# Kernel tuning notes

Hardware: AMD Instinct MI355X
Metric: run time of the kernel (lower is better)

The kernel has to match this reference:

```python
import jax, jax.numpy as jnp
import numpy as np

B, S, H, NH = 4, 1024, 2048, 32
HD = H // NH
EPS = 1e-5

def layer_norm(x, w, b):
    mu = jnp.mean(x, axis=-1, keepdims=True)
    var = jnp.mean(jnp.square(x - mu), axis=-1, keepdims=True)
    return (x - mu) * jax.lax.rsqrt(var + EPS) * w + b

def setup_inputs() -> dict:
    key = jax.random.key(0)
    ks = jax.random.split(key, 8)
    s = 0.02
    inp = {
        'hidden_states': jax.random.normal(ks[0], (B, S, H), jnp.float32),
        'mask': jnp.tril(jnp.ones((S, S), jnp.float32))[None, None],  # causal 0/1
        'ln1_w': jnp.ones((H,), jnp.float32), 'ln1_b': jnp.zeros((H,), jnp.float32),
        'w_qkv': s * jax.random.normal(ks[1], (H, 3 * H), jnp.float32),
        'b_qkv': jnp.zeros((3 * H,), jnp.float32),
        'w_dense': s * jax.random.normal(ks[2], (H, H), jnp.float32),
        'b_dense': jnp.zeros((H,), jnp.float32),
        'ln3_w': jnp.ones((H,), jnp.float32), 'ln3_b': jnp.zeros((H,), jnp.float32),
        'ln2_w': jnp.ones((H,), jnp.float32), 'ln2_b': jnp.zeros((H,), jnp.float32),
        'w_h4h': s * jax.random.normal(ks[3], (H, 4 * H), jnp.float32),
        'b_h4h': jnp.zeros((4 * H,), jnp.float32),
        'w_4hh': s * jax.random.normal(ks[4], (4 * H, H), jnp.float32),
        'b_4hh': jnp.zeros((H,), jnp.float32),
        'ln4_w': jnp.ones((H,), jnp.float32), 'ln4_b': jnp.zeros((H,), jnp.float32),
    }
    return inp

def _layer(hidden_states, mask, ln1_w, ln1_b, w_qkv, b_qkv, w_dense, b_dense,
           ln3_w, ln3_b, ln2_w, ln2_b, w_h4h, b_h4h, w_4hh, b_4hh, ln4_w, ln4_b):
    # --- input LN ---
    x1 = layer_norm(hidden_states, ln1_w, ln1_b)
    # --- self attention ---
    qkv = x1 @ w_qkv + b_qkv                              # [B,S,3H]
    q, k, v = jnp.split(qkv, 3, axis=-1)
    def heads(t):  # [B,S,H] -> [B,NH,S,HD]
        return t.reshape(B, S, NH, HD).transpose(0, 2, 1, 3)
    q, k, v = heads(q), heads(k), heads(v)
    scores = jnp.einsum('bnqd,bnkd->bnqk', q / jnp.sqrt(jnp.float32(HD)), k)
    scores = scores * mask - 10000.0 * (1.0 - mask)
    probs = jax.nn.softmax(scores, axis=-1)
    ctx = jnp.einsum('bnqk,bnkd->bnqd', probs, v)
    ctx = ctx.transpose(0, 2, 1, 3).reshape(B, S, H)
    attn_out = ctx @ w_dense + b_dense
    # sandwich LN on attention output
    attn_out = layer_norm(attn_out, ln3_w, ln3_b)
    ln_input = hidden_states + attn_out
    # --- MLP ---
    x2 = layer_norm(ln_input, ln2_w, ln2_b)
    inter = jax.nn.gelu(x2 @ w_h4h + b_h4h, approximate=True)
    mlp_out = inter @ w_4hh + b_4hh
    mlp_out = layer_norm(mlp_out, ln4_w, ln4_b)
    return ln_input + mlp_out

def reference(hidden_states, mask, ln1_w, ln1_b, w_qkv, b_qkv, w_dense, b_dense,
              ln3_w, ln3_b, ln2_w, ln2_b, w_h4h, b_h4h, w_4hh, b_4hh, ln4_w, ln4_b):
    return _layer(hidden_states, mask, ln1_w, ln1_b, w_qkv, b_qkv, w_dense, b_dense,
                  ln3_w, ln3_b, ln2_w, ln2_b, w_h4h, b_h4h, w_4hh, b_4hh, ln4_w, ln4_b)
```

## Files before the change

kernel.cpp:

```cpp
#include <hip/hip_runtime.h>
#include <cstdint>
#include <cstddef>

typedef __bf16 bf16_t;
typedef __bf16 bf16x8 __attribute__((ext_vector_type(8)));
typedef float f32x4 __attribute__((ext_vector_type(4)));

#define BB 4
#define SS 1024
#define HH 2048
#define NHH 32
#define HDD 64
#define MTOK 4096
#define QKVLD 6144

static constexpr size_t OFF_WQKV   = 0;
static constexpr size_t OFF_WDENSE = 25165824;
static constexpr size_t OFF_WH4H   = 33554432;
static constexpr size_t OFF_W4HH   = 67108864;
static constexpr size_t OFF_X1     = 100663296;
static constexpr size_t OFF_QKV    = 117440512;
static constexpr size_t OFF_ATTND2 = 150994944;
static constexpr size_t OFF_VT     = 167772160;
static constexpr size_t OFF_LNIN   = 184549376;
static constexpr size_t OFF_MLP    = 218103808;
static constexpr size_t OFF_MLP2   = 0;

__device__ __forceinline__ uint16_t f2bfu(float f) {
  union { float f; uint32_t u; } v; v.f = f;
  return (uint16_t)((v.u + 0x7FFFu + ((v.u >> 16) & 1u)) >> 16);
}
__device__ __forceinline__ bf16_t f2bf(float f) {
  union { uint16_t u; bf16_t b; } o; o.u = f2bfu(f);
  return o.b;
}

__device__ __forceinline__ void g2l16(const void* g, void* l) {
  __builtin_amdgcn_global_load_lds(
      (const __attribute__((address_space(1))) void*)g,
      (__attribute__((address_space(3))) void*)l, 16, 0, 0);
}

__global__ void convert_transpose_kernel(const float* __restrict__ W, bf16_t* __restrict__ WT,
                                         int K, int N) {
  __shared__ float t[32][33];
  const int n0 = blockIdx.x * 32;
  const int k0 = blockIdx.y * 32;
  const int tx = threadIdx.x, ty = threadIdx.y;
#pragma unroll
  for (int j = 0; j < 4; ++j)
    t[ty + j * 8][tx] = W[(size_t)(k0 + ty + j * 8) * N + n0 + tx];
  __syncthreads();
#pragma unroll
  for (int j = 0; j < 4; ++j)
    WT[(size_t)(n0 + ty + j * 8) * K + k0 + tx] = f2bf(t[tx][ty + j * 8]);
}

__global__ void transpose_v_kernel(const bf16_t* __restrict__ qkv, bf16_t* __restrict__ vT) {
  __shared__ bf16_t t[32][33];
  const int s0 = blockIdx.x * 32;
  const int d0 = blockIdx.y * 32;
  const int bh = blockIdx.z;
  const int b = bh >> 5, h = bh & 31;
  const int tx = threadIdx.x, ty = threadIdx.y;
  const bf16_t* src = qkv + (size_t)b * SS * QKVLD + 2 * HH + h * HDD;
#pragma unroll
  for (int j = 0; j < 4; ++j)
    t[ty + j * 8][tx] = src[(size_t)(s0 + ty + j * 8) * QKVLD + d0 + tx];
  __syncthreads();
  bf16_t* dst = vT + (size_t)bh * HDD * SS;
#pragma unroll
  for (int j = 0; j < 4; ++j)
    dst[(size_t)(d0 + ty + j * 8) * SS + s0 + tx] = t[tx][ty + j * 8];
}

__device__ __forceinline__ void block_reduce2(float& s, float& ss) {
#pragma unroll
  for (int o = 32; o > 0; o >>= 1) {
    s += __shfl_down(s, o, 64);
    ss += __shfl_down(ss, o, 64);
  }
  __shared__ float red[8];
  const int wave = threadIdx.x >> 6;
  const int lane = threadIdx.x & 63;
  if (lane == 0) { red[wave] = s; red[4 + wave] = ss; }
  __syncthreads();
  s = red[0] + red[1] + red[2] + red[3];
  ss = red[4] + red[5] + red[6] + red[7];
  __syncthreads();
}

__device__ __forceinline__ void load8(const float* base, int tid, float* v) {
  float4 a = ((const float4*)base)[tid];
  float4 b = ((const float4*)base)[tid + 256];
  v[0] = a.x; v[1] = a.y; v[2] = a.z; v[3] = a.w;
  v[4] = b.x; v[5] = b.y; v[6] = b.z; v[7] = b.w;
}
__device__ __forceinline__ void store8f(float* base, int tid, const float* v) {
  ((float4*)base)[tid] = make_float4(v[0], v[1], v[2], v[3]);
  ((float4*)base)[tid + 256] = make_float4(v[4], v[5], v[6], v[7]);
}
__device__ __forceinline__ void store8bf(bf16_t* base, int tid, const float* v) {
  ushort4 o0 = {f2bfu(v[0]), f2bfu(v[1]), f2bfu(v[2]), f2bfu(v[3])};
  ushort4 o1 = {f2bfu(v[4]), f2bfu(v[5]), f2bfu(v[6]), f2bfu(v[7])};
  ((ushort4*)base)[tid] = o0;
  ((ushort4*)base)[tid + 256] = o1;
}
__device__ __forceinline__ void row_stats(const float* v, float& mean, float& inv) {
  float s = 0.f, ss = 0.f;
#pragma unroll
  for (int i = 0; i < 8; ++i) { s += v[i]; ss += v[i] * v[i]; }
  block_reduce2(s, ss);
  mean = s * (1.0f / 2048.0f);
  float var = ss * (1.0f / 2048.0f) - mean * mean;
  inv = rsqrtf(var + 1e-5f);
}

__global__ __launch_bounds__(256) void ln1_kernel(const float* __restrict__ x,
                                                  const float* __restrict__ w,
                                                  const float* __restrict__ b,
                                                  bf16_t* __restrict__ out) {
  const int row = blockIdx.x, tid = threadIdx.x;
  float v[8], wv[8], bv[8], o[8];
  load8(x + (size_t)row * HH, tid, v);
  float mean, inv;
  row_stats(v, mean, inv);
  load8(w, tid, wv);
  load8(b, tid, bv);
#pragma unroll
  for (int i = 0; i < 8; ++i) o[i] = (v[i] - mean) * inv * wv[i] + bv[i];
  store8bf(out + (size_t)row * HH, tid, o);
}

__global__ __launch_bounds__(256) void fuse_mid_kernel(
    const float* __restrict__ ad, const float* __restrict__ ad2,
    const float* __restrict__ hid,
    const float* __restrict__ w3, const float* __restrict__ b3,
    const float* __restrict__ w2, const float* __restrict__ b2,
    float* __restrict__ lnin, bf16_t* __restrict__ x2) {
  const int row = blockIdx.x, tid = threadIdx.x;
  float a[8], a2[8], h[8], wv[8], bv[8], l[8], o[8];
  load8(ad + (size_t)row * HH, tid, a);
  load8(ad2 + (size_t)row * HH, tid, a2);
#pragma unroll
  for (int i = 0; i < 8; ++i) a[i] += a2[i];
  float mean3, inv3;
  row_stats(a, mean3, inv3);
  load8(hid + (size_t)row * HH, tid, h);
  load8(w3, tid, wv);
  load8(b3, tid, bv);
#pragma unroll
  for (int i = 0; i < 8; ++i) l[i] = h[i] + (a[i] - mean3) * inv3 * wv[i] + bv[i];
  store8f(lnin + (size_t)row * HH, tid, l);
  float mean2, inv2;
  row_stats(l, mean2, inv2);
  load8(w2, tid, wv);
  load8(b2, tid, bv);
#pragma unroll
  for (int i = 0; i < 8; ++i) o[i] = (l[i] - mean2) * inv2 * wv[i] + bv[i];
  store8bf(x2 + (size_t)row * HH, tid, o);
}

__global__ __launch_bounds__(256) void fuse_out_kernel(
    const float* __restrict__ mlp, const float* __restrict__ mlp2,
    const float* __restrict__ lnin,
    const float* __restrict__ w4, const float* __restrict__ b4,
    float* __restrict__ out) {
  const int row = blockIdx.x, tid = threadIdx.x;
  float m[8], m2[8], l[8], wv[8], bv[8], o[8];
  load8(mlp + (size_t)row * HH, tid, m);
  load8(mlp2 + (size_t)row * HH, tid, m2);
#pragma unroll
  for (int i = 0; i < 8; ++i) m[i] += m2[i];
  float mean4, inv4;
  row_stats(m, mean4, inv4);
  load8(lnin + (size_t)row * HH, tid, l);
  load8(w4, tid, wv);
  load8(b4, tid, bv);
#pragma unroll
  for (int i = 0; i < 8; ++i) o[i] = l[i] + (m[i] - mean4) * inv4 * wv[i] + bv[i];
  store8f(out + (size_t)row * HH, tid, o);
}

#define MFMA16(a, b, cc) __builtin_amdgcn_mfma_f32_16x16x32_bf16(a, b, cc, 0, 0, 0)

#define STAGE(ISB, BUF, HALF, KT) do {                                              \
    const char* _s = ((ISB) ? bS : aS) + (size_t)(HALF) * h128 + (size_t)(KT) * 128; \
    char* _d = lds + ((ISB) ? 65536 : 0) + (BUF) * 32768 + (HALF) * 16384 +         \
               wave * 1024;                                                         \
    g2l16(_s, _d);                                                                  \
    g2l16(_s + h64, _d + 8192);                                                     \
  } while (0)

#define LDA(BUF, MQ)                                                                \
  _Pragma("unroll") for (int mf = 0; mf < 4; ++mf) {                                \
    const char* _p = aRd + (BUF) * 32768 + (MQ) * 8192 + mf * 2048;                 \
    aR[mf * 2]     = *(const bf16x8*)(_p + colK0);                                  \
    aR[mf * 2 + 1] = *(const bf16x8*)(_p + colK1);                                  \
  }

#define LDB(BR, BUF, NQ)                                                            \
  _Pragma("unroll") for (int nf = 0; nf < 2; ++nf) {                                \
    const char* _p = bRd + (BUF) * 32768 + (NQ) * 4096 + nf * 2048;                 \
    BR[nf * 2]     = *(const bf16x8*)(_p + colK0);                                  \
    BR[nf * 2 + 1] = *(const bf16x8*)(_p + colK1);                                  \
  }

#define MMA(MQ, NQ, BR)                                                             \
  _Pragma("unroll") for (int mf = 0; mf < 4; ++mf)                                  \
  _Pragma("unroll") for (int nf = 0; nf < 2; ++nf)                                  \
  _Pragma("unroll") for (int ks = 0; ks < 2; ++ks)                                  \
    acc[(MQ) * 4 + mf][(NQ) * 2 + nf] =                                             \
        MFMA16(aR[mf * 2 + ks], BR[nf * 2 + ks], acc[(MQ) * 4 + mf][(NQ) * 2 + nf]);

#define BARS()                                                                      \
  __builtin_amdgcn_s_barrier();                                                     \
  __builtin_amdgcn_s_setprio(1);

#define ENDP()                                                                      \
  __builtin_amdgcn_s_setprio(0);                                                    \
  __builtin_amdgcn_s_barrier();

template <int EPI, int SPLITK>
__global__ __launch_bounds__(512, 2) void gemm256(
    const bf16_t* __restrict__ A, const bf16_t* __restrict__ BT,
    const float* __restrict__ bias, void* __restrict__ out0, void* __restrict__ out1,
    const int M, const int N, const int Keff, const int ldK) {
  __shared__ alignas(16) char lds[131072];
  const int tid = threadIdx.x;
  const int wave = tid >> 6, lane = tid & 63;
  const int wm = wave >> 2, wn = wave & 3;
  const int c = lane & 15, g = lane >> 4;

  const int nwg = gridDim.x;
  int bid = (blockIdx.x & 7) * (nwg >> 3) + (blockIdx.x >> 3);
  const int nm = M >> 8;
  int slice = 0;
  if (SPLITK == 2) {
    const int per = nm * (N >> 8);
    slice = bid >= per;
    bid -= slice * per;
  }
  const int mt = bid % nm, nt = bid / nm;

  const size_t ldb = (size_t)ldK * 2;
  const size_t h64 = (size_t)64 * ldb;
  const size_t h128 = 2 * h64;
  const char* aPan = (const char*)A + (size_t)(mt * 256) * ldb + (size_t)(slice * Keff) * 2;
  const char* bPan = (const char*)BT + (size_t)(nt * 256) * ldb + (size_t)(slice * Keff) * 2;

  const int srow = tid >> 3;
  const int scb = ((tid & 7) << 4) ^ ((srow & 7) << 4);
  const char* aS = aPan + (size_t)srow * ldb + scb;
  const char* bS = bPan + (size_t)srow * ldb + scb;

  const int x4 = (c & 7) << 4;
  const int colK0 = (g * 16) ^ x4;
  const int colK1 = (64 + g * 16) ^ x4;
  const char* aRd = lds + wm * 16384 + c * 128;
  const char* bRd = lds + 65536 + (wn >> 1) * 16384 + ((wn & 1) * 64 + c) * 128;

  f32x4 acc[8][4] = {};
  bf16x8 aR[8], b0R[4], b1R[4];

  const int NITER = Keff >> 7;
  const int NT2 = NITER * 2;

  STAGE(1, 0, 0, 0); STAGE(1, 0, 1, 0); STAGE(0, 0, 0, 0); STAGE(0, 0, 1, 0);
  STAGE(1, 1, 0, 1); STAGE(1, 1, 1, 1);
  asm volatile("s_waitcnt vmcnt(4)" ::: "memory");
  __builtin_amdgcn_s_barrier();

  for (int it = 0; it < NITER; ++it) {
    const int ktb = 2 * it + 1;
    int kt2 = 2 * it + 2; if (kt2 >= NT2) kt2 = 0;
    int kt3 = 2 * it + 3; if (kt3 >= NT2) kt3 = 0;
    LDA(0, 0); LDB(b0R, 0, 0); STAGE(0, 1, 0, ktb);
    BARS(); MMA(0, 0, b0R); ENDP();
    LDB(b1R, 0, 1); STAGE(0, 1, 1, ktb);
    BARS(); MMA(0, 1, b1R); ENDP();
    LDA(0, 1); STAGE(1, 0, 0, kt2);
    BARS(); MMA(1, 1, b1R); ENDP();
    STAGE(1, 0, 1, kt2);
    asm volatile("s_waitcnt vmcnt(4)" ::: "memory");
    BARS(); MMA(1, 0, b0R); ENDP();
    LDA(1, 0); LDB(b0R, 1, 0); STAGE(0, 0, 0, kt2);
    BARS(); MMA(0, 0, b0R); ENDP();
    LDB(b1R, 1, 1); STAGE(0, 0, 1, kt2);
    BARS(); MMA(0, 1, b1R); ENDP();
    LDA(1, 1); STAGE(1, 1, 0, kt3);
    BARS(); MMA(1, 1, b1R); ENDP();
    STAGE(1, 1, 1, kt3);
    asm volatile("s_waitcnt vmcnt(4)" ::: "memory");
    BARS(); MMA(1, 0, b0R); ENDP();
  }

  const int rowb = mt * 256 + wm * 128 + g * 4;
  const int colb = nt * 256 + wn * 64 + c;
  if constexpr (EPI == 0) {
    float* o = (float*)(slice ? out1 : out0);
    float bvv[4];
#pragma unroll
    for (int nf = 0; nf < 4; ++nf) bvv[nf] = (slice == 0) ? bias[colb + nf * 16] : 0.0f;
#pragma unroll
    for (int mf = 0; mf < 8; ++mf) {
      const int r = rowb + mf * 16;
#pragma unroll
      for (int e = 0; e < 4; ++e) {
        float* orow = o + (size_t)(r + e) * N + colb;
#pragma unroll
        for (int nf = 0; nf < 4; ++nf)
          orow[nf * 16] = acc[mf][nf][e] + bvv[nf];
      }
    }
  } else if constexpr (EPI == 1) {
    bf16_t* o = (bf16_t*)out0;
    float bvv[4];
#pragma unroll
    for (int nf = 0; nf < 4; ++nf) bvv[nf] = bias[colb + nf * 16];
#pragma unroll
    for (int mf = 0; mf < 8; ++mf) {
      const int r = rowb + mf * 16;
#pragma unroll
      for (int e = 0; e < 4; ++e) {
        bf16_t* orow = o + (size_t)(r + e) * N + colb;
#pragma unroll
        for (int nf = 0; nf < 4; ++nf)
          orow[nf * 16] = f2bf(acc[mf][nf][e] + bvv[nf]);
      }
    }
  } else {
    bf16_t* o = (bf16_t*)out0;
    float bvv[4];
#pragma unroll
    for (int nf = 0; nf < 4; ++nf) bvv[nf] = bias[colb + nf * 16];
#pragma unroll
    for (int mf = 0; mf < 8; ++mf) {
      const int r = rowb + mf * 16;
#pragma unroll
      for (int e = 0; e < 4; ++e) {
        bf16_t* orow = o + (size_t)(r + e) * N + colb;
#pragma unroll
        for (int nf = 0; nf < 4; ++nf) {
          float u = acc[mf][nf][e] + bvv[nf];
          float cc2 = 0.7978845608f * (u + 0.044715f * u * u * u);
          float ex = __expf(2.0f * cc2);
          float th = 1.0f - 2.0f / (ex + 1.0f);
          orow[nf * 16] = f2bf(0.5f * u * (1.0f + th));
        }
      }
    }
  }
}

__global__ __launch_bounds__(512) void attn_kernel(
    const bf16_t* __restrict__ qkv, const bf16_t* __restrict__ vT,
    bf16_t* __restrict__ ctx) {
  __shared__ alignas(16) char Ksm[8192];
  __shared__ alignas(16) char Vsm[8192];
  __shared__ alignas(16) char Psm[16384];

  const int id = blockIdx.x;
  const int qt = 7 - (id >> 7);
  const int bh = id & 127;
  const int b = bh >> 5, h = bh & 31;
  const int tid = threadIdx.x;
  const int wave = tid >> 6;
  const int lane = tid & 63;
  const int q0 = qt * 128;
  const int q0w = q0 + wave * 16;
  const int c = lane & 15;
  const int g = lane >> 4;

  const bf16_t* qb = qkv + ((size_t)b * SS + q0w) * QKVLD + h * HDD;
  const bf16x8 qa0 = *(const bf16x8*)(qb + (size_t)c * QKVLD + g * 8);
  const bf16x8 qa1 = *(const bf16x8*)(qb + (size_t)c * QKVLD + 32 + g * 8);

  f32x4 o[4] = {};
  float mrow[4], lrow[4];
#pragma unroll
  for (int e = 0; e < 4; ++e) { mrow[e] = -1e30f; lrow[e] = 0.0f; }

  const int sr = tid >> 3;
  const int sgb = ((tid & 7) * 16) ^ ((sr & 7) << 4);
  const char* kgb = (const char*)(qkv + (size_t)b * SS * QKVLD + HH + h * HDD);
  const char* vgb = (const char*)(vT + (size_t)bh * HDD * SS);
  char* kdst = Ksm + wave * 1024;
  char* vdst = Vsm + wave * 1024;
  char* Pw = Psm + wave * 2048;

  const int ntiles = (q0 + 128) >> 6;

  for (int t = 0; t < ntiles; ++t) {
    const int kb = t * 64;
    g2l16(kgb + (size_t)(kb + sr) * (QKVLD * 2) + sgb, kdst);
    g2l16(vgb + (size_t)sr * 2048 + (size_t)kb * 2 + sgb, vdst);
    __syncthreads();

    if (kb < q0w + 16) {
      f32x4 s[4] = {};
#pragma unroll
      for (int sub = 0; sub < 4; ++sub) {
        const int n = sub * 16 + c;
        const int x = (n & 7) << 4;
        bf16x8 kf0 = *(const bf16x8*)(Ksm + n * 128 + ((g * 16) ^ x));
        bf16x8 kf1 = *(const bf16x8*)(Ksm + n * 128 + ((64 + g * 16) ^ x));
        s[sub] = MFMA16(qa0, kf0, s[sub]);
        s[sub] = MFMA16(qa1, kf1, s[sub]);
      }
      const bool diag = (kb + 63 > q0w);
      float pv[4][4];
#pragma unroll
      for (int sub = 0; sub < 4; ++sub)
#pragma unroll
        for (int e = 0; e < 4; ++e) {
          float sv = s[sub][e] * 0.125f;
          if (diag && (kb + sub * 16 + c > q0w + g * 4 + e)) sv = -10000.0f;
          pv[sub][e] = sv;
        }
      float scale[4];
#pragma unroll
      for (int e = 0; e < 4; ++e) {
        float mx = fmaxf(fmaxf(pv[0][e], pv[1][e]), fmaxf(pv[2][e], pv[3][e]));
        mx = fmaxf(mx, __shfl_xor(mx, 1, 64));
        mx = fmaxf(mx, __shfl_xor(mx, 2, 64));
        mx = fmaxf(mx, __shfl_xor(mx, 4, 64));
        mx = fmaxf(mx, __shfl_xor(mx, 8, 64));
        const float mnew = fmaxf(mrow[e], mx);
        scale[e] = __expf(mrow[e] - mnew);
        mrow[e] = mnew;
      }
#pragma unroll
      for (int e = 0; e < 4; ++e) {
        const int row = g * 4 + e;
        const int xr = (row & 7) << 4;
        float sum = 0.0f;
#pragma unroll
        for (int sub = 0; sub < 4; ++sub) {
          float p = __expf(pv[sub][e] - mrow[e]);
          sum += p;
          const int cb = (sub * 16 + c) * 2;
          *(bf16_t*)(Pw + row * 128 + (cb ^ xr)) = f2bf(p);
        }
        sum += __shfl_xor(sum, 1, 64);
        sum += __shfl_xor(sum, 2, 64);
        sum += __shfl_xor(sum, 4, 64);
        sum += __shfl_xor(sum, 8, 64);
        lrow[e] = lrow[e] * scale[e] + sum;
      }
#pragma unroll
      for (int d = 0; d < 4; ++d)
#pragma unroll
        for (int e = 0; e < 4; ++e) o[d][e] *= scale[e];
      const int xa = (c & 7) << 4;
      bf16x8 pa0 = *(const bf16x8*)(Pw + c * 128 + ((g * 16) ^ xa));
      bf16x8 pa1 = *(const bf16x8*)(Pw + c * 128 + ((64 + g * 16) ^ xa));
#pragma unroll
      for (int d = 0; d < 4; ++d) {
        const int n = d * 16 + c;
        const int xv = (n & 7) << 4;
        bf16x8 vf0 = *(const bf16x8*)(Vsm + n * 128 + ((g * 16) ^ xv));
        bf16x8 vf1 = *(const bf16x8*)(Vsm + n * 128 + ((64 + g * 16) ^ xv));
        o[d] = MFMA16(pa0, vf0, o[d]);
        o[d] = MFMA16(pa1, vf1, o[d]);
      }
    }
    __syncthreads();
  }

#pragma unroll
  for (int e = 0; e < 4; ++e) {
    const int qrow = q0w + g * 4 + e;
    const float inv = 1.0f / lrow[e];
#pragma unroll
    for (int d = 0; d < 4; ++d)
      ctx[((size_t)b * SS + qrow) * HH + h * 64 + d * 16 + c] = f2bf(o[d][e] * inv);
  }
}

extern "C" void kernel_launch(void* const* d_in, const int* in_sizes, int n_in,
                              void* d_out, int out_size, void* d_ws, size_t ws_size,
                              hipStream_t stream) {
  const float* hidden = (const float*)d_in[0];
  const float* ln1w = (const float*)d_in[2];
  const float* ln1b = (const float*)d_in[3];
  const float* wqkv = (const float*)d_in[4];
  const float* bqkv = (const float*)d_in[5];
  const float* wdense = (const float*)d_in[6];
  const float* bdense = (const float*)d_in[7];
  const float* ln3w = (const float*)d_in[8];
  const float* ln3b = (const float*)d_in[9];
  const float* ln2w = (const float*)d_in[10];
  const float* ln2b = (const float*)d_in[11];
  const float* wh4h = (const float*)d_in[12];
  const float* bh4h = (const float*)d_in[13];
  const float* w4hh = (const float*)d_in[14];
  const float* b4hh = (const float*)d_in[15];
  const float* ln4w = (const float*)d_in[16];
  const float* ln4b = (const float*)d_in[17];

  char* ws = (char*)d_ws;
  bf16_t* wqkvT = (bf16_t*)(ws + OFF_WQKV);
  bf16_t* wdenseT = (bf16_t*)(ws + OFF_WDENSE);
  bf16_t* wh4hT = (bf16_t*)(ws + OFF_WH4H);
  bf16_t* w4hhT = (bf16_t*)(ws + OFF_W4HH);
  bf16_t* x1 = (bf16_t*)(ws + OFF_X1);
  bf16_t* qkv = (bf16_t*)(ws + OFF_QKV);
  bf16_t* vT = (bf16_t*)(ws + OFF_VT);
  bf16_t* ctx = (bf16_t*)(ws + OFF_X1);
  float* attnd = (float*)(ws + OFF_QKV);
  float* attnd2 = (float*)(ws + OFF_ATTND2);
  float* lnin = (float*)(ws + OFF_LNIN);
  bf16_t* x2 = (bf16_t*)(ws + OFF_X1);
  bf16_t* inter = (bf16_t*)(ws + OFF_QKV);
  float* mlp = (float*)(ws + OFF_MLP);
  float* mlp2 = (float*)(ws + OFF_MLP2);

  dim3 tb(32, 8);
  convert_transpose_kernel<<<dim3(6144 / 32, 2048 / 32), tb, 0, stream>>>(wqkv, wqkvT, 2048, 6144);
  convert_transpose_kernel<<<dim3(2048 / 32, 2048 / 32), tb, 0, stream>>>(wdense, wdenseT, 2048, 2048);
  convert_transpose_kernel<<<dim3(8192 / 32, 2048 / 32), tb, 0, stream>>>(wh4h, wh4hT, 2048, 8192);
  convert_transpose_kernel<<<dim3(2048 / 32, 8192 / 32), tb, 0, stream>>>(w4hh, w4hhT, 8192, 2048);

  ln1_kernel<<<MTOK, 256, 0, stream>>>(hidden, ln1w, ln1b, x1);

  gemm256<1, 1><<<dim3((6144 / 256) * (4096 / 256)), 512, 0, stream>>>(
      x1, wqkvT, bqkv, (void*)qkv, nullptr, MTOK, 6144, 2048, 2048);

  transpose_v_kernel<<<dim3(SS / 32, HDD / 32, BB * NHH), tb, 0, stream>>>(qkv, vT);

  attn_kernel<<<dim3(1024), 512, 0, stream>>>(qkv, vT, ctx);

  gemm256<0, 2><<<dim3((2048 / 256) * (4096 / 256) * 2), 512, 0, stream>>>(
      ctx, wdenseT, bdense, (void*)attnd, (void*)attnd2, MTOK, 2048, 1024, 2048);

  fuse_mid_kernel<<<MTOK, 256, 0, stream>>>(attnd, attnd2, hidden, ln3w, ln3b, ln2w, ln2b, lnin, x2);

  gemm256<2, 1><<<dim3((8192 / 256) * (4096 / 256)), 512, 0, stream>>>(
      x2, wh4hT, bh4h, (void*)inter, nullptr, MTOK, 8192, 2048, 2048);

  gemm256<0, 2><<<dim3((2048 / 256) * (4096 / 256) * 2), 512, 0, stream>>>(
      inter, w4hhT, b4hh, (void*)mlp, (void*)mlp2, MTOK, 2048, 4096, 8192);

  fuse_out_kernel<<<MTOK, 256, 0, stream>>>(mlp, mlp2, lnin, ln4w, ln4b, (float*)d_out);
}
```

Before: 615.4 us.

## Store split-K partials in bf16, merge weight conversions, tighten GEMM scheduling barriers

The split-K GEMM partial outputs (dense and 4h->h) are now written as bf16 instead of fp32, and the fused LN kernels read them back as bf16. This halves the write and read traffic for those intermediates, at the cost of extra rounding before the layer norms. The four weight convert-transpose launches are merged into a single launch. Scheduling barriers and an explicit lgkmcnt wait are added around the GEMM phase barriers to constrain instruction reordering.

```diff
diff --git a/kernel.cpp b/kernel.cpp
--- a/kernel.cpp
+++ b/kernel.cpp
@@ -24,7 +24,7 @@
 static constexpr size_t OFF_VT     = 167772160;
 static constexpr size_t OFF_LNIN   = 184549376;
 static constexpr size_t OFF_MLP    = 218103808;
-static constexpr size_t OFF_MLP2   = 0;
+static constexpr size_t OFF_MLP2   = 234881024;
 
 __device__ __forceinline__ uint16_t f2bfu(float f) {
   union { float f; uint32_t u; } v; v.f = f;
@@ -33,6 +33,10 @@
 __device__ __forceinline__ bf16_t f2bf(float f) {
   union { uint16_t u; bf16_t b; } o; o.u = f2bfu(f);
   return o.b;
+}
+__device__ __forceinline__ float bfu2f(uint16_t u) {
+  union { uint32_t u; float f; } v; v.u = ((uint32_t)u) << 16;
+  return v.f;
 }
 
 __device__ __forceinline__ void g2l16(const void* g, void* l) {
@@ -41,11 +45,19 @@
       (__attribute__((address_space(3))) void*)l, 16, 0, 0);
 }
 
-__global__ void convert_transpose_kernel(const float* __restrict__ W, bf16_t* __restrict__ WT,
-                                         int K, int N) {
+__global__ void convert_all_kernel(const float* __restrict__ w0, bf16_t* __restrict__ o0,
+                                   const float* __restrict__ w1, bf16_t* __restrict__ o1,
+                                   const float* __restrict__ w2, bf16_t* __restrict__ o2,
+                                   const float* __restrict__ w3, bf16_t* __restrict__ o3) {
   __shared__ float t[32][33];
-  const int n0 = blockIdx.x * 32;
-  const int k0 = blockIdx.y * 32;
+  int id = blockIdx.x;
+  const float* W; bf16_t* WT; int K, N, nt, idx;
+  if (id < 12288)      { W = w0; WT = o0; K = 2048; N = 6144; nt = 192; idx = id; }
+  else if (id < 16384) { W = w1; WT = o1; K = 2048; N = 2048; nt = 64;  idx = id - 12288; }
+  else if (id < 32768) { W = w2; WT = o2; K = 2048; N = 8192; nt = 256; idx = id - 16384; }
+  else                 { W = w3; WT = o3; K = 8192; N = 2048; nt = 64;  idx = id - 32768; }
+  const int n0 = (idx % nt) * 32;
+  const int k0 = (idx / nt) * 32;
   const int tx = threadIdx.x, ty = threadIdx.y;
 #pragma unroll
   for (int j = 0; j < 4; ++j)
@@ -95,6 +107,12 @@
   float4 b = ((const float4*)base)[tid + 256];
   v[0] = a.x; v[1] = a.y; v[2] = a.z; v[3] = a.w;
   v[4] = b.x; v[5] = b.y; v[6] = b.z; v[7] = b.w;
+}
+__device__ __forceinline__ void load8bf(const bf16_t* base, int tid, float* v) {
+  ushort4 a = ((const ushort4*)base)[tid];
+  ushort4 b = ((const ushort4*)base)[tid + 256];
+  v[0] = bfu2f(a.x); v[1] = bfu2f(a.y); v[2] = bfu2f(a.z); v[3] = bfu2f(a.w);
+  v[4] = bfu2f(b.x); v[5] = bfu2f(b.y); v[6] = bfu2f(b.z); v[7] = bfu2f(b.w);
 }
 __device__ __forceinline__ void store8f(float* base, int tid, const float* v) {
   ((float4*)base)[tid] = make_float4(v[0], v[1], v[2], v[3]);
@@ -133,15 +151,15 @@
 }
 
 __global__ __launch_bounds__(256) void fuse_mid_kernel(
-    const float* __restrict__ ad, const float* __restrict__ ad2,
+    const bf16_t* __restrict__ ad, const bf16_t* __restrict__ ad2,
     const float* __restrict__ hid,
     const float* __restrict__ w3, const float* __restrict__ b3,
     const float* __restrict__ w2, const float* __restrict__ b2,
     float* __restrict__ lnin, bf16_t* __restrict__ x2) {
   const int row = blockIdx.x, tid = threadIdx.x;
   float a[8], a2[8], h[8], wv[8], bv[8], l[8], o[8];
-  load8(ad + (size_t)row * HH, tid, a);
-  load8(ad2 + (size_t)row * HH, tid, a2);
+  load8bf(ad + (size_t)row * HH, tid, a);
+  load8bf(ad2 + (size_t)row * HH, tid, a2);
 #pragma unroll
   for (int i = 0; i < 8; ++i) a[i] += a2[i];
   float mean3, inv3;
@@ -162,14 +180,14 @@
 }
 
 __global__ __launch_bounds__(256) void fuse_out_kernel(
-    const float* __restrict__ mlp, const float* __restrict__ mlp2,
+    const bf16_t* __restrict__ mlp, const bf16_t* __restrict__ mlp2,
     const float* __restrict__ lnin,
     const float* __restrict__ w4, const float* __restrict__ b4,
     float* __restrict__ out) {
   const int row = blockIdx.x, tid = threadIdx.x;
   float m[8], m2[8], l[8], wv[8], bv[8], o[8];
-  load8(mlp + (size_t)row * HH, tid, m);
-  load8(mlp2 + (size_t)row * HH, tid, m2);
+  load8bf(mlp + (size_t)row * HH, tid, m);
+  load8bf(mlp2 + (size_t)row * HH, tid, m2);
 #pragma unroll
   for (int i = 0; i < 8; ++i) m[i] += m2[i];
   float mean4, inv4;
@@ -214,11 +232,15 @@
         MFMA16(aR[mf * 2 + ks], BR[nf * 2 + ks], acc[(MQ) * 4 + mf][(NQ) * 2 + nf]);
 
 #define BARS()                                                                      \
+  __builtin_amdgcn_sched_barrier(0);                                                \
   __builtin_amdgcn_s_barrier();                                                     \
+  asm volatile("s_waitcnt lgkmcnt(0)" ::: "memory");                                \
+  __builtin_amdgcn_sched_barrier(0);                                                \
   __builtin_amdgcn_s_setprio(1);
 
 #define ENDP()                                                                      \
   __builtin_amdgcn_s_setprio(0);                                                    \
+  __builtin_amdgcn_sched_barrier(0);                                                \
   __builtin_amdgcn_s_barrier();
 
 template <int EPI, int SPLITK>
@@ -298,7 +320,7 @@
   const int rowb = mt * 256 + wm * 128 + g * 4;
   const int colb = nt * 256 + wn * 64 + c;
   if constexpr (EPI == 0) {
-    float* o = (float*)(slice ? out1 : out0);
+    bf16_t* o = (bf16_t*)(slice ? out1 : out0);
     float bvv[4];
 #pragma unroll
     for (int nf = 0; nf < 4; ++nf) bvv[nf] = (slice == 0) ? bias[colb + nf * 16] : 0.0f;
@@ -307,10 +329,10 @@
       const int r = rowb + mf * 16;
 #pragma unroll
       for (int e = 0; e < 4; ++e) {
-        float* orow = o + (size_t)(r + e) * N + colb;
+        bf16_t* orow = o + (size_t)(r + e) * N + colb;
 #pragma unroll
         for (int nf = 0; nf < 4; ++nf)
-          orow[nf * 16] = acc[mf][nf][e] + bvv[nf];
+          orow[nf * 16] = f2bf(acc[mf][nf][e] + bvv[nf]);
       }
     }
   } else if constexpr (EPI == 1) {
@@ -508,19 +530,17 @@
   bf16_t* qkv = (bf16_t*)(ws + OFF_QKV);
   bf16_t* vT = (bf16_t*)(ws + OFF_VT);
   bf16_t* ctx = (bf16_t*)(ws + OFF_X1);
-  float* attnd = (float*)(ws + OFF_QKV);
-  float* attnd2 = (float*)(ws + OFF_ATTND2);
+  bf16_t* attnd = (bf16_t*)(ws + OFF_QKV);
+  bf16_t* attnd2 = (bf16_t*)(ws + OFF_ATTND2);
   float* lnin = (float*)(ws + OFF_LNIN);
   bf16_t* x2 = (bf16_t*)(ws + OFF_X1);
   bf16_t* inter = (bf16_t*)(ws + OFF_QKV);
-  float* mlp = (float*)(ws + OFF_MLP);
-  float* mlp2 = (float*)(ws + OFF_MLP2);
+  bf16_t* mlp = (bf16_t*)(ws + OFF_MLP);
+  bf16_t* mlp2 = (bf16_t*)(ws + OFF_MLP2);
 
   dim3 tb(32, 8);
-  convert_transpose_kernel<<<dim3(6144 / 32, 2048 / 32), tb, 0, stream>>>(wqkv, wqkvT, 2048, 6144);
-  convert_transpose_kernel<<<dim3(2048 / 32, 2048 / 32), tb, 0, stream>>>(wdense, wdenseT, 2048, 2048);
-  convert_transpose_kernel<<<dim3(8192 / 32, 2048 / 32), tb, 0, stream>>>(wh4h, wh4hT, 2048, 8192);
-  convert_transpose_kernel<<<dim3(2048 / 32, 8192 / 32), tb, 0, stream>>>(w4hh, w4hhT, 8192, 2048);
+  convert_all_kernel<<<dim3(49152), tb, 0, stream>>>(wqkv, wqkvT, wdense, wdenseT,
+                                                     wh4h, wh4hT, w4hh, w4hhT);
 
   ln1_kernel<<<MTOK, 256, 0, stream>>>(hidden, ln1w, ln1b, x1);
 
```

Measured after the change: 594.3 us. -3.4%, faster.
